# Optimization experiments

Hardware: AMD Instinct MI355X
Metric: run time of the kernel (lower is better)

The kernel has to match this reference:

```python
import jax, jax.numpy as jnp
import numpy as np

H = 4096        # hidden_size
NH = 32         # num query heads
NKV = 8         # num kv heads
HD = H // NH    # head_dim = 128
T_PREV = 16383  # cached tokens; new token makes T = 16384
BASE = 10000.0


def _rope(x, pos):
    # x: [heads, head_dim]; interleaved even/odd RoPE at a single position
    d = x.shape[-1]
    inv_freq = 1.0 / (BASE ** (jnp.arange(0, d, 2, dtype=jnp.float32) / d))
    f = pos * inv_freq                      # [d/2]
    c, s = jnp.cos(f), jnp.sin(f)
    xe, xo = x[..., 0::2], x[..., 1::2]
    out = jnp.stack([xe * c - xo * s, xe * s + xo * c], axis=-1)
    return out.reshape(x.shape)


def setup_inputs() -> dict:
    key = jax.random.key(0)
    ks = jax.random.split(key, 7)
    w = 0.02  # weight scale for numerical stability
    return {
        "hidden": jax.random.normal(ks[0], (H,), jnp.float32),
        "k_cache": jax.random.normal(ks[1], (T_PREV, NKV, HD), jnp.float32),
        "v_cache": jax.random.normal(ks[2], (T_PREV, NKV, HD), jnp.float32),
        "Wq": jax.random.normal(ks[3], (H, H), jnp.float32) * w,
        "Wk": jax.random.normal(ks[4], (NKV * HD, H), jnp.float32) * w,
        "Wv": jax.random.normal(ks[5], (NKV * HD, H), jnp.float32) * w,
        "Wo": jax.random.normal(ks[6], (H, H), jnp.float32) * w,
        "position_id": T_PREV,
    }


def reference(hidden, k_cache, v_cache, Wq, Wk, Wv, Wo, position_id):
    pos = jnp.float32(position_id)
    # projections (nn.Linear: y = W @ x), single token
    q = (Wq @ hidden).reshape(NH, HD)
    k = (Wk @ hidden).reshape(NKV, HD)
    v = (Wv @ hidden).reshape(NKV, HD)
    # inline RoPE on new q and k
    q = _rope(q, pos)
    k = _rope(k, pos)
    # contiguous KV including the new token
    k_all = jnp.concatenate([k_cache, k[None]], axis=0)   # [T, NKV, HD]
    v_all = jnp.concatenate([v_cache, v[None]], axis=0)
    # GQA: repeat KV heads to match query heads
    rep = NH // NKV
    k_all = jnp.repeat(k_all, rep, axis=1)                 # [T, NH, HD]
    v_all = jnp.repeat(v_all, rep, axis=1)
    # single-query attention
    scores = jnp.einsum('hd,thd->ht', q, k_all) / jnp.sqrt(jnp.float32(HD))
    attn = jax.nn.softmax(scores, axis=-1)                 # [NH, T]
    ctx = jnp.einsum('ht,thd->hd', attn, v_all)            # [NH, HD]
    # combine heads + output projection
    return Wo @ ctx.reshape(H)
```

## Files before the change

kernel.cpp:

```cpp
#include <hip/hip_runtime.h>
#include <math.h>

#define NH 32
#define NKV 8
#define HD 128
#define HDIM 4096
#define KVDIM 1024
#define TPREV 16383
#define NCHUNK 128
#define CHUNK 128

#define OFF_Q 0
#define OFF_K 4096
#define OFF_V 5120
#define OFF_PART 6144
#define PART_STRIDE 130
#define OFF_CTX (OFF_PART + NH * NCHUNK * PART_STRIDE)

__device__ __forceinline__ float wave_reduce_sum(float v) {
#pragma unroll
  for (int m = 32; m >= 1; m >>= 1) v += __shfl_xor(v, m, 64);
  return v;
}
__device__ __forceinline__ float wave_reduce_max(float v) {
#pragma unroll
  for (int m = 32; m >= 1; m >>= 1) v = fmaxf(v, __shfl_xor(v, m, 64));
  return v;
}
__device__ __forceinline__ float dot4(float4 a, float4 b) {
  return a.x * b.x + a.y * b.y + a.z * b.z + a.w * b.w;
}

__global__ __launch_bounds__(256) void qkv_rope_kernel(
    const float* __restrict__ Wq, const float* __restrict__ Wk,
    const float* __restrict__ Wv, const float* __restrict__ hidden,
    const int* __restrict__ pos_p, float* __restrict__ ws) {
  int r = blockIdx.x * 4 + (threadIdx.x >> 6);
  int lane = threadIdx.x & 63;
  const float* W;
  int wr;
  if (r < HDIM) {
    W = Wq; wr = r;
  } else if (r < HDIM + KVDIM) {
    W = Wk; wr = r - HDIM;
  } else {
    W = Wv; wr = r - HDIM - KVDIM;
  }
  const float4* w4 = (const float4*)(W + (size_t)wr * HDIM);
  const float4* h4 = (const float4*)hidden;
  float s = 0.f;
#pragma unroll
  for (int base = 0; base < 16; base += 8) {
    float4 a[8], b[8];
#pragma unroll
    for (int j = 0; j < 8; ++j) a[j] = w4[lane + 64 * (base + j)];
#pragma unroll
    for (int j = 0; j < 8; ++j) b[j] = h4[lane + 64 * (base + j)];
#pragma unroll
    for (int j = 0; j < 8; ++j) s += dot4(a[j], b[j]);
  }
  s = wave_reduce_sum(s);
  __shared__ float rs[4];
  if (lane == 0) rs[threadIdx.x >> 6] = s;
  __syncthreads();
  if (threadIdx.x < 2) {
    int r0 = blockIdx.x * 4 + (int)threadIdx.x * 2;
    float S0 = rs[threadIdx.x * 2], S1 = rs[threadIdx.x * 2 + 1];
    if (r0 < HDIM + KVDIM) {
      int j = (r0 & (HD - 1)) >> 1;
      double lowp = 1.0;
      if (j & 1) lowp *= 0.8659643233600653;
      if (j & 2) lowp *= 0.7498942093324559;
      if (j & 4) lowp *= 0.5623413251903491;
      if (j & 8) lowp *= 0.31622776601683794;
      double hi = (j & 16) ? 0.1 : 1.0;
      if (j & 32) hi *= 0.01;
      double f = (double)(*pos_p) * (lowp * hi);
      double k2 = floor(f * 0.15915494309189535);
      double rr = f - k2 * 6.283185307179586;
      float fr = (float)rr;
      float c = cosf(fr), sn = sinf(fr);
      ws[r0] = S0 * c - S1 * sn;
      ws[r0 + 1] = S0 * sn + S1 * c;
    } else {
      ws[r0] = S0;
      ws[r0 + 1] = S1;
    }
  }
}

__global__ __launch_bounds__(256, 4) void attn_chunk_kernel(
    const float* __restrict__ k_cache, const float* __restrict__ v_cache,
    float* __restrict__ ws) {
  int g = blockIdx.x >> 7;
  int c = blockIdx.x & 127;
  int t0 = c * CHUNK;
  int tid = threadIdx.x;

  __shared__ float qs[4 * HD];
  __shared__ float sc[CHUNK * 5];
  __shared__ float vacc[8][4][HD];
  __shared__ float wredm[4][4], wredl[4][4];
  __shared__ float mh[4], lh[4];

  for (int i = tid; i < 4 * HD; i += 256) qs[i] = ws[OFF_Q + g * 4 * HD + i];
  __syncthreads();

  const float rscale = 0.08838834764831845f;

  int itok = tid >> 1;
  int hf = tid & 1;
  int tok = t0 + itok;
  bool valid = tok < TPREV;
  float s0 = -1e30f, s1 = -1e30f, s2 = -1e30f, s3 = -1e30f;
  if (valid) {
    const float4* kp =
        (const float4*)(k_cache + (size_t)tok * KVDIM + g * HD + hf * 64);
    const float4* q4 = (const float4*)qs;
    s0 = 0.f; s1 = 0.f; s2 = 0.f; s3 = 0.f;
#pragma unroll
    for (int base = 0; base < 16; base += 8) {
      float4 kk[8];
#pragma unroll
      for (int j = 0; j < 8; ++j) kk[j] = kp[base + j];
#pragma unroll
      for (int j = 0; j < 8; ++j) {
        int qi = hf * 16 + base + j;
        s0 += dot4(kk[j], q4[0 * 32 + qi]);
        s1 += dot4(kk[j], q4[1 * 32 + qi]);
        s2 += dot4(kk[j], q4[2 * 32 + qi]);
        s3 += dot4(kk[j], q4[3 * 32 + qi]);
      }
    }
  }
  s0 += __shfl_xor(s0, 1, 64);
  s1 += __shfl_xor(s1, 1, 64);
  s2 += __shfl_xor(s2, 1, 64);
  s3 += __shfl_xor(s3, 1, 64);
  s0 *= rscale; s1 *= rscale; s2 *= rscale; s3 *= rscale;

  float m0 = wave_reduce_max(s0), m1 = wave_reduce_max(s1);
  float m2 = wave_reduce_max(s2), m3 = wave_reduce_max(s3);
  if ((tid & 63) == 0) {
    int w = tid >> 6;
    wredm[w][0] = m0; wredm[w][1] = m1; wredm[w][2] = m2; wredm[w][3] = m3;
  }
  __syncthreads();
  if (tid < 4)
    mh[tid] = fmaxf(fmaxf(wredm[0][tid], wredm[1][tid]),
                    fmaxf(wredm[2][tid], wredm[3][tid]));
  __syncthreads();

  float e0 = expf(s0 - mh[0]), e1 = expf(s1 - mh[1]);
  float e2 = expf(s2 - mh[2]), e3 = expf(s3 - mh[3]);
  if (hf == 0) {
    sc[itok * 5 + 0] = e0;
    sc[itok * 5 + 1] = e1;
    sc[itok * 5 + 2] = e2;
    sc[itok * 5 + 3] = e3;
  }
  float l0 = 0.5f * wave_reduce_sum(e0), l1 = 0.5f * wave_reduce_sum(e1);
  float l2 = 0.5f * wave_reduce_sum(e2), l3 = 0.5f * wave_reduce_sum(e3);
  if ((tid & 63) == 0) {
    int w = tid >> 6;
    wredl[w][0] = l0; wredl[w][1] = l1; wredl[w][2] = l2; wredl[w][3] = l3;
  }
  __syncthreads();
  if (tid < 4)
    lh[tid] = wredl[0][tid] + wredl[1][tid] + wredl[2][tid] + wredl[3][tid];
  __syncthreads();

  int grp = tid >> 5, lane = tid & 31;
  float4 a0 = {0, 0, 0, 0}, a1 = {0, 0, 0, 0}, a2 = {0, 0, 0, 0},
         a3 = {0, 0, 0, 0};
  const float4 z4 = {0, 0, 0, 0};
#pragma unroll
  for (int base = 0; base < 16; base += 4) {
    float4 vv[4];
#pragma unroll
    for (int j = 0; j < 4; ++j) {
      int it = grp + 8 * (base + j);
      int t = t0 + it;
      vv[j] = (t < TPREV)
                  ? ((const float4*)(v_cache + (size_t)t * KVDIM + g * HD))[lane]
                  : z4;
    }
#pragma unroll
    for (int j = 0; j < 4; ++j) {
      int it = grp + 8 * (base + j);
      float p0 = sc[it * 5 + 0], p1 = sc[it * 5 + 1];
      float p2 = sc[it * 5 + 2], p3 = sc[it * 5 + 3];
      a0.x = fmaf(p0, vv[j].x, a0.x); a0.y = fmaf(p0, vv[j].y, a0.y);
      a0.z = fmaf(p0, vv[j].z, a0.z); a0.w = fmaf(p0, vv[j].w, a0.w);
      a1.x = fmaf(p1, vv[j].x, a1.x); a1.y = fmaf(p1, vv[j].y, a1.y);
      a1.z = fmaf(p1, vv[j].z, a1.z); a1.w = fmaf(p1, vv[j].w, a1.w);
      a2.x = fmaf(p2, vv[j].x, a2.x); a2.y = fmaf(p2, vv[j].y, a2.y);
      a2.z = fmaf(p2, vv[j].z, a2.z); a2.w = fmaf(p2, vv[j].w, a2.w);
      a3.x = fmaf(p3, vv[j].x, a3.x); a3.y = fmaf(p3, vv[j].y, a3.y);
      a3.z = fmaf(p3, vv[j].z, a3.z); a3.w = fmaf(p3, vv[j].w, a3.w);
    }
  }
  ((float4*)&vacc[grp][0][0])[lane] = a0;
  ((float4*)&vacc[grp][1][0])[lane] = a1;
  ((float4*)&vacc[grp][2][0])[lane] = a2;
  ((float4*)&vacc[grp][3][0])[lane] = a3;
  __syncthreads();

  float* part = ws + OFF_PART;
#pragma unroll
  for (int rep = 0; rep < 2; ++rep) {
    int p = tid + rep * 256;
    int h = p >> 7, d = p & 127;
    float s = 0.f;
#pragma unroll
    for (int g2 = 0; g2 < 8; ++g2) s += vacc[g2][h][d];
    part[(size_t)((g * 4 + h) * NCHUNK + c) * PART_STRIDE + d] = s;
  }
  if (tid < 4) {
    part[(size_t)((g * 4 + tid) * NCHUNK + c) * PART_STRIDE + 128] = mh[tid];
    part[(size_t)((g * 4 + tid) * NCHUNK + c) * PART_STRIDE + 129] = lh[tid];
  }
}

__global__ __launch_bounds__(256) void combine_kernel(float* __restrict__ ws) {
  int h = blockIdx.x;
  int g = h >> 2;
  int tid = threadIdx.x;
  const float rscale = 0.08838834764831845f;
  const float* ph = ws + OFF_PART + (size_t)h * NCHUNK * PART_STRIDE;

  __shared__ float red[HD];
  __shared__ float wexp[NCHUNK];
  __shared__ float wm[4], wl[4];
  __shared__ float acc2[HD];

  if (tid < HD) red[tid] = ws[OFF_Q + h * HD + tid] * ws[OFF_K + g * HD + tid];
  __syncthreads();
#pragma unroll
  for (int s2 = 64; s2 >= 1; s2 >>= 1) {
    if (tid < s2 && tid + s2 < HD) red[tid] += red[tid + s2];
    __syncthreads();
  }
  float snew = red[0] * rscale;

  float mv = (tid < NCHUNK) ? ph[(size_t)tid * PART_STRIDE + 128] : -1e30f;
  float lv = (tid < NCHUNK) ? ph[(size_t)tid * PART_STRIDE + 129] : 0.f;
  float mw = wave_reduce_max(mv);
  if ((tid & 63) == 0) wm[tid >> 6] = mw;
  __syncthreads();
  float M = fmaxf(fmaxf(fmaxf(wm[0], wm[1]), fmaxf(wm[2], wm[3])), snew);
  float w = expf(mv - M);
  if (tid < NCHUNK) wexp[tid] = w;
  float lw = wave_reduce_sum(lv * w);
  if ((tid & 63) == 0) wl[tid >> 6] = lw;
  __syncthreads();
  float en = expf(snew - M);
  float L = wl[0] + wl[1] + wl[2] + wl[3] + en;

  int half = tid >> 7, d = tid & 127;
  float acc = 0.f;
  int cbeg = half * (NCHUNK / 2);
#pragma unroll 8
  for (int c2 = cbeg; c2 < cbeg + NCHUNK / 2; ++c2)
    acc = fmaf(ph[(size_t)c2 * PART_STRIDE + d], wexp[c2], acc);
  if (half == 0) acc2[d] = acc;
  __syncthreads();
  if (half == 1) acc2[d] += acc;
  __syncthreads();
  if (tid < HD)
    ws[OFF_CTX + h * HD + tid] =
        (acc2[tid] + en * ws[OFF_V + g * HD + tid]) / L;
}

__global__ __launch_bounds__(256) void out_matvec_kernel(
    const float* __restrict__ Wo, const float* __restrict__ ws,
    float* __restrict__ out) {
  int r = blockIdx.x * 4 + (threadIdx.x >> 6);
  int lane = threadIdx.x & 63;
  const float4* w4 = (const float4*)(Wo + (size_t)r * HDIM);
  const float4* x4 = (const float4*)(ws + OFF_CTX);
  float s = 0.f;
#pragma unroll
  for (int base = 0; base < 16; base += 8) {
    float4 a[8], b[8];
#pragma unroll
    for (int j = 0; j < 8; ++j) a[j] = w4[lane + 64 * (base + j)];
#pragma unroll
    for (int j = 0; j < 8; ++j) b[j] = x4[lane + 64 * (base + j)];
#pragma unroll
    for (int j = 0; j < 8; ++j) s += dot4(a[j], b[j]);
  }
  s = wave_reduce_sum(s);
  if (lane == 0) out[r] = s;
}

extern "C" void kernel_launch(void* const* d_in, const int* in_sizes, int n_in,
                              void* d_out, int out_size, void* d_ws,
                              size_t ws_size, hipStream_t stream) {
  const float* hidden = (const float*)d_in[0];
  const float* k_cache = (const float*)d_in[1];
  const float* v_cache = (const float*)d_in[2];
  const float* Wq = (const float*)d_in[3];
  const float* Wk = (const float*)d_in[4];
  const float* Wv = (const float*)d_in[5];
  const float* Wo = (const float*)d_in[6];
  const int* pos = (const int*)d_in[7];
  float* out = (float*)d_out;
  float* ws = (float*)d_ws;

  qkv_rope_kernel<<<(HDIM + 2 * KVDIM) / 4, 256, 0, stream>>>(Wq, Wk, Wv,
                                                              hidden, pos, ws);
  attn_chunk_kernel<<<NKV * NCHUNK, 256, 0, stream>>>(k_cache, v_cache, ws);
  combine_kernel<<<NH, 256, 0, stream>>>(ws);
  out_matvec_kernel<<<HDIM / 4, 256, 0, stream>>>(Wo, ws, out);
}
```

Measured before the change: 292.8 us.

## Stage KV chunks into LDS via async global_load_lds with double-phase pipelining

```diff
diff --git a/kernel.cpp b/kernel.cpp
--- a/kernel.cpp
+++ b/kernel.cpp
@@ -1,5 +1,6 @@
 #include <hip/hip_runtime.h>
 #include <math.h>
+#include <stdint.h>
 
 #define NH 32
 #define NKV 8
@@ -9,12 +10,13 @@
 #define TPREV 16383
 #define NCHUNK 128
 #define CHUNK 128
+#define PTOK 64
 
 #define OFF_Q 0
 #define OFF_K 4096
 #define OFF_V 5120
 #define OFF_PART 6144
-#define PART_STRIDE 130
+#define PART_STRIDE 132
 #define OFF_CTX (OFF_PART + NH * NCHUNK * PART_STRIDE)
 
 __device__ __forceinline__ float wave_reduce_sum(float v) {
@@ -30,6 +32,20 @@
 __device__ __forceinline__ float dot4(float4 a, float4 b) {
   return a.x * b.x + a.y * b.y + a.z * b.z + a.w * b.w;
 }
+
+typedef const __attribute__((address_space(1))) unsigned int* gld_gp;
+typedef __attribute__((address_space(3))) unsigned int* gld_lp;
+__device__ __forceinline__ void cp16(const float* g, float* l) {
+  __builtin_amdgcn_global_load_lds((gld_gp)(uintptr_t)g,
+                                   (gld_lp)(uint32_t)(uintptr_t)l, 16, 0, 0);
+}
+
+#define BAR_LGKM()                                       \
+  do {                                                   \
+    asm volatile("s_waitcnt lgkmcnt(0)" ::: "memory");   \
+    __builtin_amdgcn_s_barrier();                        \
+    asm volatile("" ::: "memory");                       \
+  } while (0)
 
 __global__ __launch_bounds__(256) void qkv_rope_kernel(
     const float* __restrict__ Wq, const float* __restrict__ Wk,
@@ -89,136 +105,190 @@
   }
 }
 
-__global__ __launch_bounds__(256, 4) void attn_chunk_kernel(
+__global__ __launch_bounds__(256, 2) void attn_chunk_kernel(
     const float* __restrict__ k_cache, const float* __restrict__ v_cache,
     float* __restrict__ ws) {
   int g = blockIdx.x >> 7;
   int c = blockIdx.x & 127;
   int t0 = c * CHUNK;
   int tid = threadIdx.x;
-
-  __shared__ float qs[4 * HD];
-  __shared__ float sc[CHUNK * 5];
-  __shared__ float vacc[8][4][HD];
+  int l = tid & 63, w = tid >> 6;
+
+  __shared__ __align__(16) float Klds[PTOK * HD];
+  __shared__ __align__(16) float Vlds[PTOK * HD];
+  __shared__ __align__(16) float qs[4 * HD];
+  __shared__ float sc[PTOK * 5];
+  __shared__ float rm[4], rl[4], wold[4];
   __shared__ float wredm[4][4], wredl[4][4];
-  __shared__ float mh[4], lh[4];
-
-  for (int i = tid; i < 4 * HD; i += 256) qs[i] = ws[OFF_Q + g * 4 * HD + i];
-  __syncthreads();
+
+  if (tid < 4) { rm[tid] = -1e30f; rl[tid] = 0.f; }
+
+  if (w < 2)
+    cp16(ws + OFF_Q + (g << 9) + (w << 8) + (l << 2), qs + (w << 8));
+#pragma unroll
+  for (int i = 0; i < 8; ++i) {
+    int tokA = (w << 4) + 2 * i;
+    int toks = tokA + (l >> 5);
+    int gt = t0 + toks;
+    if (gt >= TPREV) gt = 0;
+    cp16(k_cache + (size_t)gt * KVDIM + g * HD + (((l & 31) ^ (toks & 7)) << 2),
+         Klds + (tokA << 7));
+  }
+#pragma unroll
+  for (int i = 0; i < 8; ++i) {
+    int tokA = (w << 4) + 2 * i;
+    int toks = tokA + (l >> 5);
+    int gt = t0 + toks;
+    if (gt >= TPREV) gt = 0;
+    cp16(v_cache + (size_t)gt * KVDIM + g * HD + ((l & 31) << 2),
+         Vlds + (tokA << 7));
+  }
+  asm volatile("s_waitcnt vmcnt(8) lgkmcnt(0)" ::: "memory");
+  __builtin_amdgcn_s_barrier();
+  asm volatile("" ::: "memory");
 
   const float rscale = 0.08838834764831845f;
-
-  int itok = tid >> 1;
-  int hf = tid & 1;
-  int tok = t0 + itok;
-  bool valid = tok < TPREV;
-  float s0 = -1e30f, s1 = -1e30f, s2 = -1e30f, s3 = -1e30f;
-  if (valid) {
-    const float4* kp =
-        (const float4*)(k_cache + (size_t)tok * KVDIM + g * HD + hf * 64);
-    const float4* q4 = (const float4*)qs;
-    s0 = 0.f; s1 = 0.f; s2 = 0.f; s3 = 0.f;
-#pragma unroll
-    for (int base = 0; base < 16; base += 8) {
-      float4 kk[8];
-#pragma unroll
-      for (int j = 0; j < 8; ++j) kk[j] = kp[base + j];
-#pragma unroll
-      for (int j = 0; j < 8; ++j) {
-        int qi = hf * 16 + base + j;
-        s0 += dot4(kk[j], q4[0 * 32 + qi]);
-        s1 += dot4(kk[j], q4[1 * 32 + qi]);
-        s2 += dot4(kk[j], q4[2 * 32 + qi]);
-        s3 += dot4(kk[j], q4[3 * 32 + qi]);
+  int tokl = (w << 4) + (l & 15);
+  int qq = l >> 4;
+  int t7 = tokl & 7;
+  int grp8 = tid >> 5, d4 = tid & 31;
+  float4 acc0 = {0, 0, 0, 0}, acc1 = {0, 0, 0, 0};
+  float4 acc2 = {0, 0, 0, 0}, acc3 = {0, 0, 0, 0};
+  const float4* K4 = (const float4*)Klds;
+  const float4* q4 = (const float4*)qs;
+  const float4* V4 = (const float4*)Vlds;
+
+#pragma unroll
+  for (int p = 0; p < 2; ++p) {
+    float s0 = 0.f, s1 = 0.f, s2 = 0.f, s3 = 0.f;
+#pragma unroll
+    for (int j = 0; j < 8; ++j) {
+      float4 kk = K4[(tokl << 5) + (qq << 3) + (j ^ t7)];
+      float4 qa = q4[0 * 32 + (qq << 3) + j];
+      float4 qb = q4[1 * 32 + (qq << 3) + j];
+      float4 qc = q4[2 * 32 + (qq << 3) + j];
+      float4 qd_ = q4[3 * 32 + (qq << 3) + j];
+      s0 += dot4(kk, qa); s1 += dot4(kk, qb);
+      s2 += dot4(kk, qc); s3 += dot4(kk, qd_);
+    }
+    s0 += __shfl_xor(s0, 16, 64); s0 += __shfl_xor(s0, 32, 64);
+    s1 += __shfl_xor(s1, 16, 64); s1 += __shfl_xor(s1, 32, 64);
+    s2 += __shfl_xor(s2, 16, 64); s2 += __shfl_xor(s2, 32, 64);
+    s3 += __shfl_xor(s3, 16, 64); s3 += __shfl_xor(s3, 32, 64);
+    s0 *= rscale; s1 *= rscale; s2 *= rscale; s3 *= rscale;
+    if (t0 + p * PTOK + tokl >= TPREV) {
+      s0 = -1e30f; s1 = -1e30f; s2 = -1e30f; s3 = -1e30f;
+    }
+
+    float m0 = wave_reduce_max(s0), m1 = wave_reduce_max(s1);
+    float m2 = wave_reduce_max(s2), m3 = wave_reduce_max(s3);
+    if (l == 0) {
+      wredm[w][0] = m0; wredm[w][1] = m1; wredm[w][2] = m2; wredm[w][3] = m3;
+    }
+    BAR_LGKM();
+    if (p == 0) {
+#pragma unroll
+      for (int i = 0; i < 8; ++i) {
+        int tokA = (w << 4) + 2 * i;
+        int toks = tokA + (l >> 5);
+        int gt = t0 + PTOK + toks;
+        if (gt >= TPREV) gt = 0;
+        cp16(k_cache + (size_t)gt * KVDIM + g * HD +
+                 (((l & 31) ^ (toks & 7)) << 2),
+             Klds + (tokA << 7));
       }
     }
-  }
-  s0 += __shfl_xor(s0, 1, 64);
-  s1 += __shfl_xor(s1, 1, 64);
-  s2 += __shfl_xor(s2, 1, 64);
-  s3 += __shfl_xor(s3, 1, 64);
-  s0 *= rscale; s1 *= rscale; s2 *= rscale; s3 *= rscale;
-
-  float m0 = wave_reduce_max(s0), m1 = wave_reduce_max(s1);
-  float m2 = wave_reduce_max(s2), m3 = wave_reduce_max(s3);
-  if ((tid & 63) == 0) {
-    int w = tid >> 6;
-    wredm[w][0] = m0; wredm[w][1] = m1; wredm[w][2] = m2; wredm[w][3] = m3;
-  }
-  __syncthreads();
-  if (tid < 4)
-    mh[tid] = fmaxf(fmaxf(wredm[0][tid], wredm[1][tid]),
-                    fmaxf(wredm[2][tid], wredm[3][tid]));
-  __syncthreads();
-
-  float e0 = expf(s0 - mh[0]), e1 = expf(s1 - mh[1]);
-  float e2 = expf(s2 - mh[2]), e3 = expf(s3 - mh[3]);
-  if (hf == 0) {
-    sc[itok * 5 + 0] = e0;
-    sc[itok * 5 + 1] = e1;
-    sc[itok * 5 + 2] = e2;
-    sc[itok * 5 + 3] = e3;
-  }
-  float l0 = 0.5f * wave_reduce_sum(e0), l1 = 0.5f * wave_reduce_sum(e1);
-  float l2 = 0.5f * wave_reduce_sum(e2), l3 = 0.5f * wave_reduce_sum(e3);
-  if ((tid & 63) == 0) {
-    int w = tid >> 6;
-    wredl[w][0] = l0; wredl[w][1] = l1; wredl[w][2] = l2; wredl[w][3] = l3;
-  }
-  __syncthreads();
-  if (tid < 4)
-    lh[tid] = wredl[0][tid] + wredl[1][tid] + wredl[2][tid] + wredl[3][tid];
-  __syncthreads();
-
-  int grp = tid >> 5, lane = tid & 31;
-  float4 a0 = {0, 0, 0, 0}, a1 = {0, 0, 0, 0}, a2 = {0, 0, 0, 0},
-         a3 = {0, 0, 0, 0};
-  const float4 z4 = {0, 0, 0, 0};
-#pragma unroll
-  for (int base = 0; base < 16; base += 4) {
-    float4 vv[4];
-#pragma unroll
-    for (int j = 0; j < 4; ++j) {
-      int it = grp + 8 * (base + j);
-      int t = t0 + it;
-      vv[j] = (t < TPREV)
-                  ? ((const float4*)(v_cache + (size_t)t * KVDIM + g * HD))[lane]
-                  : z4;
-    }
-#pragma unroll
-    for (int j = 0; j < 4; ++j) {
-      int it = grp + 8 * (base + j);
-      float p0 = sc[it * 5 + 0], p1 = sc[it * 5 + 1];
-      float p2 = sc[it * 5 + 2], p3 = sc[it * 5 + 3];
-      a0.x = fmaf(p0, vv[j].x, a0.x); a0.y = fmaf(p0, vv[j].y, a0.y);
-      a0.z = fmaf(p0, vv[j].z, a0.z); a0.w = fmaf(p0, vv[j].w, a0.w);
-      a1.x = fmaf(p1, vv[j].x, a1.x); a1.y = fmaf(p1, vv[j].y, a1.y);
-      a1.z = fmaf(p1, vv[j].z, a1.z); a1.w = fmaf(p1, vv[j].w, a1.w);
-      a2.x = fmaf(p2, vv[j].x, a2.x); a2.y = fmaf(p2, vv[j].y, a2.y);
-      a2.z = fmaf(p2, vv[j].z, a2.z); a2.w = fmaf(p2, vv[j].w, a2.w);
-      a3.x = fmaf(p3, vv[j].x, a3.x); a3.y = fmaf(p3, vv[j].y, a3.y);
-      a3.z = fmaf(p3, vv[j].z, a3.z); a3.w = fmaf(p3, vv[j].w, a3.w);
-    }
-  }
-  ((float4*)&vacc[grp][0][0])[lane] = a0;
-  ((float4*)&vacc[grp][1][0])[lane] = a1;
-  ((float4*)&vacc[grp][2][0])[lane] = a2;
-  ((float4*)&vacc[grp][3][0])[lane] = a3;
-  __syncthreads();
-
-  float* part = ws + OFF_PART;
-#pragma unroll
-  for (int rep = 0; rep < 2; ++rep) {
-    int p = tid + rep * 256;
-    int h = p >> 7, d = p & 127;
-    float s = 0.f;
-#pragma unroll
-    for (int g2 = 0; g2 < 8; ++g2) s += vacc[g2][h][d];
-    part[(size_t)((g * 4 + h) * NCHUNK + c) * PART_STRIDE + d] = s;
+    if (tid < 4) {
+      float mh = fmaxf(fmaxf(wredm[0][tid], wredm[1][tid]),
+                       fmaxf(wredm[2][tid], wredm[3][tid]));
+      float M = fmaxf(rm[tid], mh);
+      wold[tid] = expf(rm[tid] - M);
+      rm[tid] = M;
+    }
+    BAR_LGKM();
+
+    float M0 = rm[0], M1 = rm[1], M2 = rm[2], M3 = rm[3];
+    float w0 = wold[0], w1 = wold[1], w2 = wold[2], w3 = wold[3];
+    acc0.x *= w0; acc0.y *= w0; acc0.z *= w0; acc0.w *= w0;
+    acc1.x *= w1; acc1.y *= w1; acc1.z *= w1; acc1.w *= w1;
+    acc2.x *= w2; acc2.y *= w2; acc2.z *= w2; acc2.w *= w2;
+    acc3.x *= w3; acc3.y *= w3; acc3.z *= w3; acc3.w *= w3;
+
+    float e0 = expf(s0 - M0), e1 = expf(s1 - M1);
+    float e2 = expf(s2 - M2), e3 = expf(s3 - M3);
+    if (qq == 0) {
+      sc[tokl * 5 + 0] = e0; sc[tokl * 5 + 1] = e1;
+      sc[tokl * 5 + 2] = e2; sc[tokl * 5 + 3] = e3;
+    }
+    float l0 = 0.25f * wave_reduce_sum(e0), l1 = 0.25f * wave_reduce_sum(e1);
+    float l2 = 0.25f * wave_reduce_sum(e2), l3 = 0.25f * wave_reduce_sum(e3);
+    if (l == 0) {
+      wredl[w][0] = l0; wredl[w][1] = l1; wredl[w][2] = l2; wredl[w][3] = l3;
+    }
+    if (p == 0)
+      asm volatile("s_waitcnt vmcnt(8) lgkmcnt(0)" ::: "memory");
+    else
+      asm volatile("s_waitcnt vmcnt(0) lgkmcnt(0)" ::: "memory");
+    __builtin_amdgcn_s_barrier();
+    asm volatile("" ::: "memory");
+    if (tid < 4)
+      rl[tid] = rl[tid] * wold[tid] + wredl[0][tid] + wredl[1][tid] +
+                wredl[2][tid] + wredl[3][tid];
+
+#pragma unroll
+    for (int t = 0; t < 8; ++t) {
+      int tok = (grp8 << 3) + t;
+      float4 vv = V4[(tok << 5) + d4];
+      float p0_ = sc[tok * 5 + 0], p1_ = sc[tok * 5 + 1];
+      float p2_ = sc[tok * 5 + 2], p3_ = sc[tok * 5 + 3];
+      acc0.x = fmaf(p0_, vv.x, acc0.x); acc0.y = fmaf(p0_, vv.y, acc0.y);
+      acc0.z = fmaf(p0_, vv.z, acc0.z); acc0.w = fmaf(p0_, vv.w, acc0.w);
+      acc1.x = fmaf(p1_, vv.x, acc1.x); acc1.y = fmaf(p1_, vv.y, acc1.y);
+      acc1.z = fmaf(p1_, vv.z, acc1.z); acc1.w = fmaf(p1_, vv.w, acc1.w);
+      acc2.x = fmaf(p2_, vv.x, acc2.x); acc2.y = fmaf(p2_, vv.y, acc2.y);
+      acc2.z = fmaf(p2_, vv.z, acc2.z); acc2.w = fmaf(p2_, vv.w, acc2.w);
+      acc3.x = fmaf(p3_, vv.x, acc3.x); acc3.y = fmaf(p3_, vv.y, acc3.y);
+      acc3.z = fmaf(p3_, vv.z, acc3.z); acc3.w = fmaf(p3_, vv.w, acc3.w);
+    }
+
+    if (p == 0) {
+      BAR_LGKM();
+#pragma unroll
+      for (int i = 0; i < 8; ++i) {
+        int tokA = (w << 4) + 2 * i;
+        int toks = tokA + (l >> 5);
+        int gt = t0 + PTOK + toks;
+        if (gt >= TPREV) gt = 0;
+        cp16(v_cache + (size_t)gt * KVDIM + g * HD + ((l & 31) << 2),
+             Vlds + (tokA << 7));
+      }
+      asm volatile("s_waitcnt vmcnt(8)" ::: "memory");
+    }
+  }
+
+  float4* vacc4 = (float4*)Klds;
+  vacc4[(grp8 * 4 + 0) * 32 + d4] = acc0;
+  vacc4[(grp8 * 4 + 1) * 32 + d4] = acc1;
+  vacc4[(grp8 * 4 + 2) * 32 + d4] = acc2;
+  vacc4[(grp8 * 4 + 3) * 32 + d4] = acc3;
+  BAR_LGKM();
+  if (tid < 128) {
+    int h = tid >> 5, dd = tid & 31;
+    float4 s = {0, 0, 0, 0};
+#pragma unroll
+    for (int g2 = 0; g2 < 8; ++g2) {
+      float4 v = vacc4[(g2 * 4 + h) * 32 + dd];
+      s.x += v.x; s.y += v.y; s.z += v.z; s.w += v.w;
+    }
+    float* dst = ws + OFF_PART +
+                 ((size_t)(g * 4 + h) * NCHUNK + c) * PART_STRIDE + (dd << 2);
+    *(float4*)dst = s;
   }
   if (tid < 4) {
-    part[(size_t)((g * 4 + tid) * NCHUNK + c) * PART_STRIDE + 128] = mh[tid];
-    part[(size_t)((g * 4 + tid) * NCHUNK + c) * PART_STRIDE + 129] = lh[tid];
+    float* base =
+        ws + OFF_PART + ((size_t)(g * 4 + tid) * NCHUNK + c) * PART_STRIDE;
+    base[128] = rm[tid];
+    base[129] = rl[tid];
   }
 }
 
```

After: 287.1 us. No clear change (-2.0%).
